# Optimization experiments

Measured on AMD Instinct MI355X. Metric: run time of the kernel, lower is better.

Reference implementation:

```python
import jax, jax.numpy as jnp
import numpy as np

B, N, F, L = 4, 8192, 64, 2


def setup_inputs() -> dict:
    key = jax.random.key(0)
    k1, k2, k3 = jax.random.split(key, 3)
    x = jax.random.normal(k1, (B, N, F), dtype=jnp.float32)
    net_params = jax.random.normal(k2, (L * F * F,), dtype=jnp.float32)
    A = jax.random.normal(k3, (N, N), dtype=jnp.float32)
    return {"x": x, "t": 0, "net_params": net_params, "A": A}


def reference(x, t, net_params, A):
    # weights: [L, F, F]
    weights = net_params.reshape(L, F, F)
    # x: [B, N, F] (original does x.view(-1, A.size(1), features))
    z = x.reshape(-1, A.shape[1], F)
    for i in range(L):
        # GCN_operation: Z_out = A @ Z @ W_i  (the nested vmm loops emulate exactly this)
        h = jnp.einsum('mn,bnf->bmf', A, z)          # [B, N, F]
        z = jnp.einsum('bmf,fg->bmg', h, weights[i])  # [B, N, F]
        z = jax.nn.relu(z)
    return z
```

## Files before the change

kernel.cpp:

```cpp
#include <hip/hip_runtime.h>
#include <stdint.h>


#define MK 8192

typedef float f32x4 __attribute__((ext_vector_type(4)));
typedef uint32_t u32x4 __attribute__((ext_vector_type(4)));
typedef uint32_t u32x2 __attribute__((ext_vector_type(2)));
typedef __bf16 bf16x8 __attribute__((ext_vector_type(8)));

__device__ inline uint16_t f2bf(float f) {
  uint32_t u = __builtin_bit_cast(uint32_t, f);
  u += 0x7fffu + ((u >> 16) & 1u);
  return (uint16_t)(u >> 16);
}
__device__ inline float bf2f(uint32_t lo16) {
  return __builtin_bit_cast(float, lo16 << 16);
}

#define GLD(src, dstbase)                                                                    \
  __builtin_amdgcn_global_load_lds((const __attribute__((address_space(1))) uint32_t*)(src), \
                                   (__attribute__((address_space(3))) uint32_t*)(dstbase),   \
                                   16, 0, 0)

__global__ __launch_bounds__(256) void zw0(const float* __restrict__ x,
                                           const float* __restrict__ net,
                                           uint16_t* __restrict__ Zt) {
  __shared__ float Wl[64 * 64];
  __shared__ float rows[64][65];
  const int b = blockIdx.y, n0 = blockIdx.x * 64, tid = threadIdx.x;
  for (int i = tid * 4; i < 4096; i += 1024) {
    f32x4 v = *(const f32x4*)(net + i);
    Wl[i] = v[0]; Wl[i + 1] = v[1]; Wl[i + 2] = v[2]; Wl[i + 3] = v[3];
  }
  const float* src = x + ((uint64_t)b * MK + n0) * 64;
  for (int i = tid * 4; i < 4096; i += 1024) {
    f32x4 v = *(const f32x4*)(src + i);
    int r = i >> 6, f = i & 63;
    rows[r][f] = v[0]; rows[r][f + 1] = v[1]; rows[r][f + 2] = v[2]; rows[r][f + 3] = v[3];
  }
  __syncthreads();
  const int nl = tid & 63, g0 = (tid >> 6) * 16;
  float s[16];
#pragma unroll
  for (int j = 0; j < 16; ++j) s[j] = 0.f;
  for (int f = 0; f < 64; ++f) {
    float rv = rows[nl][f];
#pragma unroll
    for (int j = 0; j < 16; ++j) s[j] = fmaf(rv, Wl[f * 64 + g0 + j], s[j]);
  }
  uint16_t* dst = Zt + (uint64_t)(b * 64 + g0) * MK + n0 + nl;
#pragma unroll
  for (int j = 0; j < 16; ++j) dst[(uint64_t)j * MK] = f2bf(s[j]);
}

__global__ __launch_bounds__(512, 1) void gemm1(const float* __restrict__ Af,
                                                const uint16_t* __restrict__ Bt,
                                                uint16_t* __restrict__ Ab,
                                                uint16_t* __restrict__ P) {
  __shared__ __align__(16) uint16_t LB[65536];
#define AS1(b) (LB + (b)*16384)
#define BS1(b) (LB + 32768 + (b)*16384)
  const int bid = (int)blockIdx.x;
  const int s = bid & 7, bm = bid >> 3;
  const int row0 = bm * 256, k0 = s * 1024;
  const int tid = threadIdx.x, wid = tid >> 6, lane = tid & 63;
  const int wr = wid >> 2, wc = wid & 3;

  const int lsub = lane >> 3;
  const int ksrc = ((lane & 7) ^ lsub) << 3;
  const uint16_t* gB0 = Bt + (uint64_t)(4 * wid * 8 + lsub) * MK + k0 + ksrc;
  const int lBo = 4 * wid * 512;

  const int arow = (8 * wid) * 4 + (lane >> 4);
  const int acol = (lane & 15) * 4;
  const float* gA0 = Af + (uint64_t)(row0 + arow) * MK + k0 + acol;
  const int koct = (lane & 15) >> 1, krem = (lane & 1) * 4;

  f32x4 acc[8][4] = {};
  f32x4 rv[8];

  auto loadA = [&](int kofs) {
#pragma unroll
    for (int j = 0; j < 8; ++j)
      rv[j] = __builtin_nontemporal_load((const f32x4*)(gA0 + (uint64_t)j * 4 * MK + kofs));
  };
  auto stageA = [&](int buf, int kofs) {
#pragma unroll
    for (int j = 0; j < 8; ++j) {
      const int r = arow + j * 4;
      u32x2 w;
      w[0] = (uint32_t)f2bf(rv[j][0]) | ((uint32_t)f2bf(rv[j][1]) << 16);
      w[1] = (uint32_t)f2bf(rv[j][2]) | ((uint32_t)f2bf(rv[j][3]) << 16);
      *(u32x2*)&AS1(buf)[r * 64 + ((koct ^ (r & 7)) << 3) + krem] = w;
      *(u32x2*)(Ab + (uint64_t)(row0 + r) * MK + k0 + kofs + acol) = w;
    }
  };

  loadA(0);
#pragma unroll
  for (int j = 0; j < 4; ++j) GLD(gB0 + (uint64_t)j * 8 * MK, &BS1(0)[lBo + j * 512]);
  stageA(0, 0);
  __syncthreads();

  int buf = 0;
  for (int t = 0; t < 16; ++t) {
    const int nxt = (t + 1) * 64;
    if (t < 15) {
      loadA(nxt);
#pragma unroll
      for (int j = 0; j < 4; ++j) GLD(gB0 + (uint64_t)j * 8 * MK + nxt, &BS1(buf ^ 1)[lBo + j * 512]);
    }
#pragma unroll
    for (int kk = 0; kk < 2; ++kk) {
      const int kb = kk * 4 + (lane >> 4);
      bf16x8 a[8], b[4];
#pragma unroll
      for (int mi = 0; mi < 8; ++mi) {
        const int r = wr * 128 + mi * 16 + (lane & 15);
        a[mi] = *(const bf16x8*)&AS1(buf)[r * 64 + ((kb ^ (r & 7)) << 3)];
      }
#pragma unroll
      for (int n = 0; n < 4; ++n) {
        const int r = wc * 64 + n * 16 + (lane & 15);
        b[n] = *(const bf16x8*)&BS1(buf)[r * 64 + ((kb ^ (r & 7)) << 3)];
      }
#pragma unroll
      for (int mi = 0; mi < 8; ++mi)
#pragma unroll
        for (int n = 0; n < 4; ++n)
          acc[mi][n] = __builtin_amdgcn_mfma_f32_16x16x32_bf16(a[mi], b[n], acc[mi][n], 0, 0, 0);
    }
    if (t < 15) stageA(buf ^ 1, nxt);
    __syncthreads();
    buf ^= 1;
  }

  __syncthreads();
  const int lr = (lane >> 4) * 4, lc = lane & 15;
#pragma unroll
  for (int mi = 0; mi < 8; ++mi)
#pragma unroll
    for (int n = 0; n < 4; ++n)
#pragma unroll
      for (int j = 0; j < 4; ++j)
        LB[(wr * 128 + mi * 16 + lr + j) * 256 + (wc * 64 + n * 16 + lc)] = f2bf(acc[mi][n][j]);
  __syncthreads();
  uint16_t* Pp = P + (uint64_t)s * 2097152 + (uint64_t)row0 * 256;
#pragma unroll
  for (int i = 0; i < 16; ++i) {
    u32x4 v = *(const u32x4*)&LB[i * 4096 + tid * 8];
    *(u32x4*)(Pp + i * 4096 + tid * 8) = v;
  }
#undef AS1
#undef BS1
}

__global__ __launch_bounds__(512, 1) void gemm2(const uint16_t* __restrict__ Ab,
                                                const uint16_t* __restrict__ Bt,
                                                uint16_t* __restrict__ P) {
  __shared__ __align__(16) uint16_t LB[65536];
#define AS2(b) (LB + (b)*16384)
#define BS2(b) (LB + 32768 + (b)*16384)
  const int bid = (int)blockIdx.x;
  const int s = bid & 7, bm = bid >> 3;
  const int row0 = bm * 256, k0 = s * 1024;
  const int tid = threadIdx.x, wid = tid >> 6, lane = tid & 63;
  const int wr = wid >> 2, wc = wid & 3;

  const int lsub = lane >> 3;
  const int ksrc = ((lane & 7) ^ lsub) << 3;
  const uint16_t* gA0 = Ab + (uint64_t)(row0 + 4 * wid * 8 + lsub) * MK + k0 + ksrc;
  const uint16_t* gB0 = Bt + (uint64_t)(4 * wid * 8 + lsub) * MK + k0 + ksrc;
  const int lo = 4 * wid * 512;

  f32x4 acc[8][4] = {};

#pragma unroll
  for (int j = 0; j < 4; ++j) {
    GLD(gA0 + (uint64_t)j * 8 * MK, &AS2(0)[lo + j * 512]);
    GLD(gB0 + (uint64_t)j * 8 * MK, &BS2(0)[lo + j * 512]);
  }

  int buf = 0;
  for (int t = 0; t < 16; ++t) {
    const int tko = ((t + 1) < 16 ? (t + 1) : 15) * 64;
#pragma unroll
    for (int j = 0; j < 4; ++j) {
      GLD(gA0 + (uint64_t)j * 8 * MK + tko, &AS2(buf ^ 1)[lo + j * 512]);
      GLD(gB0 + (uint64_t)j * 8 * MK + tko, &BS2(buf ^ 1)[lo + j * 512]);
    }
    asm volatile("s_waitcnt vmcnt(8)" ::: "memory");
    __builtin_amdgcn_s_barrier();
    __builtin_amdgcn_sched_barrier(0);

    bf16x8 b[4][2];
#pragma unroll
    for (int n = 0; n < 4; ++n)
#pragma unroll
      for (int kk = 0; kk < 2; ++kk) {
        const int r = wc * 64 + n * 16 + (lane & 15);
        const int kb = kk * 4 + (lane >> 4);
        b[n][kk] = *(const bf16x8*)&BS2(buf)[r * 64 + ((kb ^ (r & 7)) << 3)];
      }
#pragma unroll
    for (int q = 0; q < 4; ++q) {
      bf16x8 a[2][2];
#pragma unroll
      for (int i = 0; i < 2; ++i)
#pragma unroll
        for (int kk = 0; kk < 2; ++kk) {
          const int r = wr * 128 + (2 * q + i) * 16 + (lane & 15);
          const int kb = kk * 4 + (lane >> 4);
          a[i][kk] = *(const bf16x8*)&AS2(buf)[r * 64 + ((kb ^ (r & 7)) << 3)];
        }
      __builtin_amdgcn_s_setprio(1);
#pragma unroll
      for (int kk = 0; kk < 2; ++kk)
#pragma unroll
        for (int i = 0; i < 2; ++i)
#pragma unroll
          for (int n = 0; n < 4; ++n)
            acc[2 * q + i][n] =
                __builtin_amdgcn_mfma_f32_16x16x32_bf16(a[i][kk], b[n][kk], acc[2 * q + i][n], 0, 0, 0);
      __builtin_amdgcn_s_setprio(0);
      __builtin_amdgcn_sched_barrier(0);
    }
    __builtin_amdgcn_s_barrier();
    buf ^= 1;
  }

  __syncthreads();
  const int lr = (lane >> 4) * 4, lc = lane & 15;
#pragma unroll
  for (int mi = 0; mi < 8; ++mi)
#pragma unroll
    for (int n = 0; n < 4; ++n)
#pragma unroll
      for (int j = 0; j < 4; ++j)
        LB[(wr * 128 + mi * 16 + lr + j) * 256 + (wc * 64 + n * 16 + lc)] = f2bf(acc[mi][n][j]);
  __syncthreads();
  uint16_t* Pp = P + (uint64_t)s * 2097152 + (uint64_t)row0 * 256;
#pragma unroll
  for (int i = 0; i < 16; ++i) {
    u32x4 v = *(const u32x4*)&LB[i * 4096 + tid * 8];
    *(u32x4*)(Pp + i * 4096 + tid * 8) = v;
  }
#undef AS2
#undef BS2
}

__global__ __launch_bounds__(256) void zw1P(const uint16_t* __restrict__ P,
                                            const float* __restrict__ net,
                                            uint16_t* __restrict__ Zt) {
  __shared__ float Wl[64 * 64];
  __shared__ float rows[64][65];
  const int b = blockIdx.y, n0 = blockIdx.x * 64, tid = threadIdx.x;
  const float* Wsrc = net + 4096;
  for (int i = tid * 4; i < 4096; i += 1024) {
    f32x4 v = *(const f32x4*)(Wsrc + i);
    Wl[i] = v[0]; Wl[i + 1] = v[1]; Wl[i + 2] = v[2]; Wl[i + 3] = v[3];
  }
#pragma unroll
  for (int g = 0; g < 2; ++g) {
    const int idx = (tid + g * 256) * 8;
    const int r = idx >> 6, f0 = idx & 63;
    const uint16_t* base = P + (uint64_t)(n0 + r) * 256 + b * 64 + f0;
    float acc8[8] = {};
#pragma unroll
    for (int sp = 0; sp < 8; ++sp) {
      u32x4 v = *(const u32x4*)(base + (uint64_t)sp * 2097152);
#pragma unroll
      for (int j = 0; j < 4; ++j) {
        acc8[2 * j]     += bf2f(v[j] & 0xffffu);
        acc8[2 * j + 1] += bf2f(v[j] >> 16);
      }
    }
#pragma unroll
    for (int j = 0; j < 8; ++j) rows[r][f0 + j] = fmaxf(acc8[j], 0.0f);
  }
  __syncthreads();
  const int nl = tid & 63, g0 = (tid >> 6) * 16;
  float s[16];
#pragma unroll
  for (int j = 0; j < 16; ++j) s[j] = 0.f;
  for (int f = 0; f < 64; ++f) {
    float rv = rows[nl][f];
#pragma unroll
    for (int j = 0; j < 16; ++j) s[j] = fmaf(rv, Wl[f * 64 + g0 + j], s[j]);
  }
  uint16_t* dst = Zt + (uint64_t)(b * 64 + g0) * MK + n0 + nl;
#pragma unroll
  for (int j = 0; j < 16; ++j) dst[(uint64_t)j * MK] = f2bf(s[j]);
}

__global__ __launch_bounds__(256) void combineF(const uint16_t* __restrict__ P,
                                                float* __restrict__ out) {
  const uint64_t e = ((uint64_t)blockIdx.x * 256 + threadIdx.x) * 8;
  float acc8[8] = {};
#pragma unroll
  for (int sp = 0; sp < 8; ++sp) {
    u32x4 v = *(const u32x4*)&P[(uint64_t)sp * 2097152 + e];
#pragma unroll
    for (int j = 0; j < 4; ++j) {
      acc8[2 * j]     += bf2f(v[j] & 0xffffu);
      acc8[2 * j + 1] += bf2f(v[j] >> 16);
    }
  }
  const int m = (int)(e >> 8);
  const int c = (int)(e & 255);
  float* dst = &out[(((uint64_t)(c >> 6)) * MK + m) * 64 + (c & 63)];
  f32x4 w0, w1;
#pragma unroll
  for (int j = 0; j < 4; ++j) { w0[j] = fmaxf(acc8[j], 0.0f); w1[j] = fmaxf(acc8[4 + j], 0.0f); }
  *(f32x4*)dst = w0;
  *(f32x4*)(dst + 4) = w1;
}

extern "C" void kernel_launch(void* const* d_in, const int* in_sizes, int n_in,
                              void* d_out, int out_size, void* d_ws, size_t ws_size,
                              hipStream_t stream) {
  const float* x   = (const float*)d_in[0];
  const float* net = (const float*)d_in[2];
  const float* A   = (const float*)d_in[3];
  float* out = (float*)d_out;

  uint16_t* Ab = (uint16_t*)d_ws;
  uint16_t* Zt = (uint16_t*)((char*)d_ws + 134217728ull);
  uint16_t* P  = (uint16_t*)((char*)d_ws + 142606336ull);

  zw0<<<dim3(128, 4), dim3(256), 0, stream>>>(x, net, Zt);
  gemm1<<<dim3(256), dim3(512), 0, stream>>>(A, Zt, Ab, P);
  zw1P<<<dim3(128, 4), dim3(256), 0, stream>>>(P, net, Zt);
  gemm2<<<dim3(256), dim3(512), 0, stream>>>(Ab, Zt, P);
  combineF<<<dim3(1024), dim3(256), 0, stream>>>(P, out);
}
```

Baseline: 167.3 us.

## Stream fp32 A tiles directly into LDS and convert to bf16 from shared memory

gemm1 now loads the fp32 adjacency tile straight into LDS with global_load_lds DMA instead of routing it through registers. The bf16 conversion happens while reading MFMA fragments from LDS, and a separate pass writes the bf16 copy of A to global from LDS. The k-step shrinks from 64 to 32, giving 32 iterations with an explicit vmcnt wait and raw barriers. The epilogue is split into two halves to fit a larger 96KB LDS footprint. This is meant to overlap the dominant fp32 A read with compute and to cut register pressure and VALU conversion on the load path. In exchange it converts A twice, adds more LDS traffic and doubles the number of barriers.

```diff
diff --git a/kernel.cpp b/kernel.cpp
--- a/kernel.cpp
+++ b/kernel.cpp
@@ -58,102 +58,106 @@
                                                 const uint16_t* __restrict__ Bt,
                                                 uint16_t* __restrict__ Ab,
                                                 uint16_t* __restrict__ P) {
-  __shared__ __align__(16) uint16_t LB[65536];
-#define AS1(b) (LB + (b)*16384)
-#define BS1(b) (LB + 32768 + (b)*16384)
+  __shared__ __align__(16) uint8_t LBRAW[98304];
+  float* AF = (float*)LBRAW;
+  uint16_t* BSg = (uint16_t*)(LBRAW + 65536);
+  uint16_t* EP = (uint16_t*)LBRAW;
   const int bid = (int)blockIdx.x;
   const int s = bid & 7, bm = bid >> 3;
   const int row0 = bm * 256, k0 = s * 1024;
   const int tid = threadIdx.x, wid = tid >> 6, lane = tid & 63;
   const int wr = wid >> 2, wc = wid & 3;
-
-  const int lsub = lane >> 3;
-  const int ksrc = ((lane & 7) ^ lsub) << 3;
-  const uint16_t* gB0 = Bt + (uint64_t)(4 * wid * 8 + lsub) * MK + k0 + ksrc;
-  const int lBo = 4 * wid * 512;
-
-  const int arow = (8 * wid) * 4 + (lane >> 4);
-  const int acol = (lane & 15) * 4;
-  const float* gA0 = Af + (uint64_t)(row0 + arow) * MK + k0 + acol;
-  const int koct = (lane & 15) >> 1, krem = (lane & 1) * 4;
+  const int fr = lane & 15, fk = lane >> 4;
+
+  const int ac = 4 * wid, arl = lane >> 3;
+  const int aq = ((lane & 7) ^ arl) * 4;
+  const int bc = 2 * wid, brl = lane >> 2;
+  const int bq = ((lane & 3) ^ (brl & 3)) * 8;
 
   f32x4 acc[8][4] = {};
-  f32x4 rv[8];
-
-  auto loadA = [&](int kofs) {
-#pragma unroll
-    for (int j = 0; j < 8; ++j)
-      rv[j] = __builtin_nontemporal_load((const f32x4*)(gA0 + (uint64_t)j * 4 * MK + kofs));
+
+  auto stage = [&](int buf, int t) {
+    const int ko = k0 + t * 32;
+#pragma unroll
+    for (int e = 0; e < 4; ++e)
+      GLD(Af + (uint64_t)(row0 + (ac + e) * 8 + arl) * MK + ko + aq,
+          &AF[buf * 8192 + (ac + e) * 256 + lane * 4]);
+#pragma unroll
+    for (int e = 0; e < 2; ++e)
+      GLD(Bt + (uint64_t)((bc + e) * 16 + brl) * MK + ko + bq,
+          &BSg[buf * 8192 + (bc + e) * 512 + lane * 8]);
   };
-  auto stageA = [&](int buf, int kofs) {
-#pragma unroll
-    for (int j = 0; j < 8; ++j) {
-      const int r = arow + j * 4;
-      u32x2 w;
-      w[0] = (uint32_t)f2bf(rv[j][0]) | ((uint32_t)f2bf(rv[j][1]) << 16);
-      w[1] = (uint32_t)f2bf(rv[j][2]) | ((uint32_t)f2bf(rv[j][3]) << 16);
-      *(u32x2*)&AS1(buf)[r * 64 + ((koct ^ (r & 7)) << 3) + krem] = w;
-      *(u32x2*)(Ab + (uint64_t)(row0 + r) * MK + k0 + kofs + acol) = w;
-    }
-  };
-
-  loadA(0);
-#pragma unroll
-  for (int j = 0; j < 4; ++j) GLD(gB0 + (uint64_t)j * 8 * MK, &BS1(0)[lBo + j * 512]);
-  stageA(0, 0);
-  __syncthreads();
-
+
+  stage(0, 0);
   int buf = 0;
-  for (int t = 0; t < 16; ++t) {
-    const int nxt = (t + 1) * 64;
-    if (t < 15) {
-      loadA(nxt);
-#pragma unroll
-      for (int j = 0; j < 4; ++j) GLD(gB0 + (uint64_t)j * 8 * MK + nxt, &BS1(buf ^ 1)[lBo + j * 512]);
-    }
-#pragma unroll
-    for (int kk = 0; kk < 2; ++kk) {
-      const int kb = kk * 4 + (lane >> 4);
-      bf16x8 a[8], b[4];
-#pragma unroll
-      for (int mi = 0; mi < 8; ++mi) {
-        const int r = wr * 128 + mi * 16 + (lane & 15);
-        a[mi] = *(const bf16x8*)&AS1(buf)[r * 64 + ((kb ^ (r & 7)) << 3)];
+  for (int t = 0; t < 32; ++t) {
+    stage(buf ^ 1, (t + 1 < 32) ? t + 1 : 31);
+    asm volatile("s_waitcnt vmcnt(6)" ::: "memory");
+    __builtin_amdgcn_s_barrier();
+    __builtin_amdgcn_sched_barrier(0);
+
+    const float* AFb = &AF[buf * 8192];
+    const uint16_t* Bb = &BSg[buf * 8192];
+    bf16x8 bfr[4];
+#pragma unroll
+    for (int n = 0; n < 4; ++n) {
+      const int r = wc * 64 + n * 16 + fr;
+      bfr[n] = *(const bf16x8*)&Bb[r * 32 + ((fk ^ (r & 3)) << 3)];
+    }
+#pragma unroll
+    for (int mi = 0; mi < 8; ++mi) {
+      const int r = wr * 128 + mi * 16 + fr;
+      f32x4 lo = *(const f32x4*)&AFb[r * 32 + ((((2 * fk) ^ (r & 7))) << 2)];
+      f32x4 hi = *(const f32x4*)&AFb[r * 32 + ((((2 * fk + 1) ^ (r & 7))) << 2)];
+      bf16x8 a;
+#pragma unroll
+      for (int j = 0; j < 4; ++j) { a[j] = (__bf16)lo[j]; a[4 + j] = (__bf16)hi[j]; }
+#pragma unroll
+      for (int n = 0; n < 4; ++n)
+        acc[mi][n] = __builtin_amdgcn_mfma_f32_16x16x32_bf16(a, bfr[n], acc[mi][n], 0, 0, 0);
+    }
+
+    {
+      const int tr = tid >> 1, hh = tid & 1;
+      f32x4 q0 = *(const f32x4*)&AFb[tr * 32 + (((4 * hh + 0) ^ (tr & 7)) << 2)];
+      f32x4 q1 = *(const f32x4*)&AFb[tr * 32 + (((4 * hh + 1) ^ (tr & 7)) << 2)];
+      f32x4 q2 = *(const f32x4*)&AFb[tr * 32 + (((4 * hh + 2) ^ (tr & 7)) << 2)];
+      f32x4 q3 = *(const f32x4*)&AFb[tr * 32 + (((4 * hh + 3) ^ (tr & 7)) << 2)];
+      bf16x8 o0, o1;
+#pragma unroll
+      for (int j = 0; j < 4; ++j) {
+        o0[j] = (__bf16)q0[j]; o0[4 + j] = (__bf16)q1[j];
+        o1[j] = (__bf16)q2[j]; o1[4 + j] = (__bf16)q3[j];
       }
-#pragma unroll
-      for (int n = 0; n < 4; ++n) {
-        const int r = wc * 64 + n * 16 + (lane & 15);
-        b[n] = *(const bf16x8*)&BS1(buf)[r * 64 + ((kb ^ (r & 7)) << 3)];
-      }
+      uint16_t* dst = Ab + (uint64_t)(row0 + tr) * MK + k0 + t * 32 + hh * 16;
+      *(bf16x8*)dst = o0;
+      *(bf16x8*)(dst + 8) = o1;
+    }
+    __builtin_amdgcn_s_barrier();
+    buf ^= 1;
+  }
+
+  uint16_t* Pbase = P + (uint64_t)s * 2097152 + (uint64_t)row0 * 256;
+  const int lr = fk * 4, lc = fr;
+#pragma unroll
+  for (int half = 0; half < 2; ++half) {
+    __syncthreads();
+    if (wr == half) {
 #pragma unroll
       for (int mi = 0; mi < 8; ++mi)
 #pragma unroll
         for (int n = 0; n < 4; ++n)
-          acc[mi][n] = __builtin_amdgcn_mfma_f32_16x16x32_bf16(a[mi], b[n], acc[mi][n], 0, 0, 0);
-    }
-    if (t < 15) stageA(buf ^ 1, nxt);
+#pragma unroll
+          for (int j = 0; j < 4; ++j)
+            EP[(mi * 16 + lr + j) * 256 + (wc * 64 + n * 16 + lc)] = f2bf(acc[mi][n][j]);
+    }
     __syncthreads();
-    buf ^= 1;
-  }
-
-  __syncthreads();
-  const int lr = (lane >> 4) * 4, lc = lane & 15;
-#pragma unroll
-  for (int mi = 0; mi < 8; ++mi)
-#pragma unroll
-    for (int n = 0; n < 4; ++n)
-#pragma unroll
-      for (int j = 0; j < 4; ++j)
-        LB[(wr * 128 + mi * 16 + lr + j) * 256 + (wc * 64 + n * 16 + lc)] = f2bf(acc[mi][n][j]);
-  __syncthreads();
-  uint16_t* Pp = P + (uint64_t)s * 2097152 + (uint64_t)row0 * 256;
-#pragma unroll
-  for (int i = 0; i < 16; ++i) {
-    u32x4 v = *(const u32x4*)&LB[i * 4096 + tid * 8];
-    *(u32x4*)(Pp + i * 4096 + tid * 8) = v;
-  }
-#undef AS1
-#undef BS1
+#pragma unroll
+    for (int i = 0; i < 8; ++i) {
+      u32x4 v = *(const u32x4*)&EP[i * 4096 + tid * 8];
+      *(u32x4*)(Pbase + half * 32768 + i * 4096 + tid * 8) = v;
+    }
+  }
 }
 
 __global__ __launch_bounds__(512, 1) void gemm2(const uint16_t* __restrict__ Ab,
```

Result: slower. 194.6 us (+16.3%).

## Deepen A-operand prefetch to two register sets with manual waitcnt barriers

Applied to the files above, without the earlier changes.

Restructures the first GEMM's main K loop to unroll by two and alternate between two register buffers for the fp32 A tiles. A loads are issued two iterations ahead, and __syncthreads is replaced with explicit vmcnt/lgkmcnt waits and raw s_barrier plus sched_barrier. The aim is to hide global-load latency behind the MFMA work. In exchange it uses more VGPRs and performs redundant clamped loads at the tail, and the hand-tuned vmcnt count must exactly match the number of outstanding loads to stay correct.

```diff
diff --git a/kernel.cpp b/kernel.cpp
--- a/kernel.cpp
+++ b/kernel.cpp
@@ -78,14 +78,14 @@
   const int koct = (lane & 15) >> 1, krem = (lane & 1) * 4;
 
   f32x4 acc[8][4] = {};
-  f32x4 rv[8];
-
-  auto loadA = [&](int kofs) {
+  f32x4 rvE[8], rvO[8];
+
+  auto loadA = [&](f32x4 (&rv)[8], int kofs) {
 #pragma unroll
     for (int j = 0; j < 8; ++j)
       rv[j] = __builtin_nontemporal_load((const f32x4*)(gA0 + (uint64_t)j * 4 * MK + kofs));
   };
-  auto stageA = [&](int buf, int kofs) {
+  auto stageA = [&](const f32x4 (&rv)[8], int buf, int kofs) {
 #pragma unroll
     for (int j = 0; j < 8; ++j) {
       const int r = arow + j * 4;
@@ -96,21 +96,11 @@
       *(u32x2*)(Ab + (uint64_t)(row0 + r) * MK + k0 + kofs + acol) = w;
     }
   };
-
-  loadA(0);
-#pragma unroll
-  for (int j = 0; j < 4; ++j) GLD(gB0 + (uint64_t)j * 8 * MK, &BS1(0)[lBo + j * 512]);
-  stageA(0, 0);
-  __syncthreads();
-
-  int buf = 0;
-  for (int t = 0; t < 16; ++t) {
-    const int nxt = (t + 1) * 64;
-    if (t < 15) {
-      loadA(nxt);
-#pragma unroll
-      for (int j = 0; j < 4; ++j) GLD(gB0 + (uint64_t)j * 8 * MK + nxt, &BS1(buf ^ 1)[lBo + j * 512]);
-    }
+  auto stageB = [&](int buf, int kofs) {
+#pragma unroll
+    for (int j = 0; j < 4; ++j) GLD(gB0 + (uint64_t)j * 8 * MK + kofs, &BS1(buf)[lBo + j * 512]);
+  };
+  auto compute = [&](int buf) {
 #pragma unroll
     for (int kk = 0; kk < 2; ++kk) {
       const int kb = kk * 4 + (lane >> 4);
@@ -131,9 +121,36 @@
         for (int n = 0; n < 4; ++n)
           acc[mi][n] = __builtin_amdgcn_mfma_f32_16x16x32_bf16(a[mi], b[n], acc[mi][n], 0, 0, 0);
     }
-    if (t < 15) stageA(buf ^ 1, nxt);
-    __syncthreads();
-    buf ^= 1;
+  };
+
+  stageB(0, 0);
+  loadA(rvE, 0);
+  loadA(rvO, 64);
+  stageA(rvE, 0, 0);
+  asm volatile("s_waitcnt lgkmcnt(0)" ::: "memory");
+  __builtin_amdgcn_s_barrier();
+  __builtin_amdgcn_sched_barrier(0);
+
+  for (int tt = 0; tt < 16; tt += 2) {
+    stageB(1, (tt + 1) * 64);
+    loadA(rvE, (tt + 2 < 16 ? tt + 2 : 15) * 64);
+    compute(0);
+    stageA(rvO, 1, (tt + 1) * 64);
+    asm volatile("s_waitcnt vmcnt(16)" ::: "memory");
+    asm volatile("s_waitcnt lgkmcnt(0)" ::: "memory");
+    __builtin_amdgcn_s_barrier();
+    __builtin_amdgcn_sched_barrier(0);
+
+    stageB(0, (tt + 2 < 16 ? tt + 2 : 15) * 64);
+    loadA(rvO, (tt + 3 < 16 ? tt + 3 : 15) * 64);
+    compute(1);
+    if (tt + 2 < 16) {
+      stageA(rvE, 0, (tt + 2) * 64);
+      asm volatile("s_waitcnt vmcnt(16)" ::: "memory");
+      asm volatile("s_waitcnt lgkmcnt(0)" ::: "memory");
+      __builtin_amdgcn_s_barrier();
+      __builtin_amdgcn_sched_barrier(0);
+    }
   }
 
   __syncthreads();
```

Result: slower. 250.9 us (+50.0%).

## Deepen A/B prefetch pipeline with explicit vmcnt waits and raw barriers

Applied to the files above, without the earlier changes.

Restructures the GEMM main loop into a deeper software pipeline: register loads of A run two tiles ahead, while B's global-to-LDS loads and A's LDS staging run one tile ahead. A __syncthreads is replaced by hand-placed s_waitcnt vmcnt(16)/lgkmcnt(0) plus s_barrier and sched_barrier, so outstanding global loads can stay in flight across iterations. This aims to hide global memory latency behind MFMA work. In exchange, tail iterations clamp the prefetch index to tile 15 and redundantly reload and restage it, and correctness now depends on hand-counted vmcnt values.

```diff
diff --git a/kernel.cpp b/kernel.cpp
--- a/kernel.cpp
+++ b/kernel.cpp
@@ -96,21 +96,11 @@
       *(u32x2*)(Ab + (uint64_t)(row0 + r) * MK + k0 + kofs + acol) = w;
     }
   };
-
-  loadA(0);
-#pragma unroll
-  for (int j = 0; j < 4; ++j) GLD(gB0 + (uint64_t)j * 8 * MK, &BS1(0)[lBo + j * 512]);
-  stageA(0, 0);
-  __syncthreads();
-
-  int buf = 0;
-  for (int t = 0; t < 16; ++t) {
-    const int nxt = (t + 1) * 64;
-    if (t < 15) {
-      loadA(nxt);
-#pragma unroll
-      for (int j = 0; j < 4; ++j) GLD(gB0 + (uint64_t)j * 8 * MK + nxt, &BS1(buf ^ 1)[lBo + j * 512]);
-    }
+  auto stageB = [&](int buf, int kofs) {
+#pragma unroll
+    for (int j = 0; j < 4; ++j) GLD(gB0 + (uint64_t)j * 8 * MK + kofs, &BS1(buf)[lBo + j * 512]);
+  };
+  auto compute = [&](int buf) {
 #pragma unroll
     for (int kk = 0; kk < 2; ++kk) {
       const int kb = kk * 4 + (lane >> 4);
@@ -131,8 +121,29 @@
         for (int n = 0; n < 4; ++n)
           acc[mi][n] = __builtin_amdgcn_mfma_f32_16x16x32_bf16(a[mi], b[n], acc[mi][n], 0, 0, 0);
     }
-    if (t < 15) stageA(buf ^ 1, nxt);
-    __syncthreads();
+  };
+
+  loadA(0);
+  stageB(0, 0);
+  stageA(0, 0);
+  loadA(64);
+  asm volatile("s_waitcnt vmcnt(16)" ::: "memory");
+  asm volatile("s_waitcnt lgkmcnt(0)" ::: "memory");
+  __builtin_amdgcn_s_barrier();
+  __builtin_amdgcn_sched_barrier(0);
+
+  int buf = 0;
+  for (int t = 0; t < 16; ++t) {
+    const int nk = (t + 1 < 16 ? t + 1 : 15) * 64;
+    const int pk = (t + 2 < 16 ? t + 2 : 15) * 64;
+    stageB(buf ^ 1, nk);
+    stageA(buf ^ 1, nk);
+    loadA(pk);
+    compute(buf);
+    asm volatile("s_waitcnt vmcnt(16)" ::: "memory");
+    asm volatile("s_waitcnt lgkmcnt(0)" ::: "memory");
+    __builtin_amdgcn_s_barrier();
+    __builtin_amdgcn_sched_barrier(0);
     buf ^= 1;
   }
 
```

New measurement: 176.6 us. 1.06x slower.
